# Kernel optimization log

Measured on AMD Instinct MI355X. Metric: run time of the kernel, lower is better.

Reference implementation:

```python
import jax, jax.numpy as jnp
import numpy as np

B, S, N, H, F, L, Lt = 2, 8, 150, 128, 40, 2, 1
EF = 2 * F + 2  # 82: src feat + dst feat + distance + bond
_rows_np, _cols_np = np.where(~np.eye(N, dtype=bool))  # fully connected, no self loops
_rows = jnp.asarray(_rows_np)
_cols = jnp.asarray(_cols_np)
E = _rows_np.shape[0]


def setup_inputs() -> dict:
    key = jax.random.key(0)
    ks = jax.random.split(key, 20)
    w = lambda k, shape: 0.1 * jax.random.normal(k, shape, dtype=jnp.float32)
    d = {}
    d['t'] = jax.random.uniform(ks[0], (B, 1), dtype=jnp.float32)
    d['x'] = jax.random.normal(ks[1], (B, S, N, 3), dtype=jnp.float32)
    d['peptide_seq'] = jax.random.randint(ks[2], (B, 15), 0, 20)
    d['atom_labels'] = jax.random.randint(ks[3], (B, N), 0, 5)
    d['amino_acid_pos'] = jax.random.randint(ks[4], (B, N), 1, 16)
    d['bond_matrix'] = (jax.random.uniform(ks[5], (B, N, N)) < 0.1).astype(jnp.float32)
    d['edge_mask'] = jnp.ones((B, N, N), jnp.float32)
    d['atom_mask'] = jnp.ones((B, N, 1), jnp.float32)
    d['restore_indices'] = jnp.tile(jnp.eye(N, dtype=jnp.float32)[None], (B, 1, 1))
    d['W_e1'] = w(ks[6], (L, EF, H)); d['b_e1'] = jnp.zeros((L, H), jnp.float32)
    d['W_e2'] = w(ks[7], (L, H, H)); d['b_e2'] = jnp.zeros((L, H), jnp.float32)
    d['W_c'] = w(ks[8], (L, H, 1)); d['b_c'] = jnp.zeros((L, 1), jnp.float32)
    d['W_h'] = w(ks[9], (L, F + H, F)); d['b_h'] = jnp.zeros((L, F), jnp.float32)
    d['w_t'] = w(ks[10], (L, 1, H)); d['w_b_t'] = jnp.zeros((L, H), jnp.float32)
    d['tW_e1'] = w(ks[11], (Lt, EF, H)); d['tb_e1'] = jnp.zeros((Lt, H), jnp.float32)
    d['tW_e2'] = w(ks[12], (Lt, H, H)); d['tb_e2'] = jnp.zeros((Lt, H), jnp.float32)
    d['tW_c'] = w(ks[13], (Lt, H, 1)); d['tb_c'] = jnp.zeros((Lt, 1), jnp.float32)
    d['tW_h'] = w(ks[14], (Lt, F + H, F)); d['tb_h'] = jnp.zeros((Lt, F), jnp.float32)
    return d


def _forward(t, x, peptide_seq, atom_labels, amino_acid_pos, bond_matrix, edge_mask,
             atom_mask, restore_indices, W_e1, b_e1, W_e2, b_e2, W_c, b_c, W_h, b_h,
             w_t, w_b_t, tW_e1, tb_e1, tW_e2, tb_e2, tW_c, tb_c, tW_h, tb_h):
    # single-atom embedding: [B, N, 40]
    aa = jnp.take_along_axis(peptide_seq, amino_acid_pos - 1, axis=1)
    emb = jnp.concatenate([
        jax.nn.one_hot(atom_labels, 5, dtype=x.dtype),
        jax.nn.one_hot(aa, 20, dtype=x.dtype),
        jax.nn.one_hot(amino_acid_pos - 1, 15, dtype=x.dtype)], axis=-1)
    h = jnp.broadcast_to(emb[:, None], (B, S, N, F))
    # restore absolute coordinates: x[b,s,i,d] = sum_j x[b,s,j,d] * R[b,i,j]
    x = jnp.einsum('bsjd,bij->bsid', x, restore_indices)
    x0 = x
    # per-edge masks/features (gathered once; identical math to full cdist + indexing)
    em_e = edge_mask.reshape(B, 1, N * N)[:, :, _rows * N + _cols][..., None]  # [B,1,E,1]
    bond_e = jnp.broadcast_to(bond_matrix[:, _rows, _cols][:, None, :, None], (B, S, E, 1))

    def layer(x, h, We1, be1, We2, be2, Wc, bc, Wh, bh, temb):
        diff = x[:, :, _rows] - x[:, :, _cols]                      # [B,S,E,3]
        dist = jnp.sqrt(jnp.sum(diff * diff, -1, keepdims=True) + 1e-12)
        ef = jnp.concatenate([h[:, :, _rows], h[:, :, _cols], dist, bond_e], -1)  # [B,S,E,82]
        m = jax.nn.silu(ef @ We1 + be1 + temb)
        m = jax.nn.silu(m @ We2 + be2) * em_e                        # [B,S,E,H]
        cw = m @ Wc + bc                                             # [B,S,E,1]
        x_out = jnp.zeros_like(x).at[:, :, _rows].add(diff * cw) / (N - 1)
        agg = jnp.zeros((B, S, N, m.shape[-1]), m.dtype).at[:, :, _rows].add(m)
        h_out = jax.nn.silu(jnp.concatenate([h, agg], -1) @ Wh + bh)
        return x_out, h_out

    for l in range(L):
        temb = (t @ w_t[l] + w_b_t[l])[:, None, None, :]             # [B,1,1,H]
        xo, h = layer(x, h, W_e1[l], b_e1[l], W_e2[l], b_e2[l], W_c[l], b_c[l], W_h[l], b_h[l], temb)
        x = x + xo
    for l in range(Lt):
        xo, h = layer(x, h, tW_e1[l], tb_e1[l], tW_e2[l], tb_e2[l], tW_c[l], tb_c[l], tW_h[l], tb_h[l], 0.0)
        x = x + xo
    return (x - x0) * atom_mask[:, None, :, :]


def reference(t, x, peptide_seq, atom_labels, amino_acid_pos, bond_matrix, edge_mask,
              atom_mask, restore_indices, W_e1, b_e1, W_e2, b_e2, W_c, b_c, W_h, b_h,
              w_t, w_b_t, tW_e1, tb_e1, tW_e2, tb_e2, tW_c, tb_c, tW_h, tb_h):
    return _forward(t, x, peptide_seq, atom_labels, amino_acid_pos, bond_matrix, edge_mask,
                    atom_mask, restore_indices, W_e1, b_e1, W_e2, b_e2, W_c, b_c, W_h, b_h,
                    w_t, w_b_t, tW_e1, tb_e1, tW_e2, tb_e2, tW_c, tb_c, tW_h, tb_h)
```

## Files before the change

### kernel.cpp

```cpp
#include <hip/hip_runtime.h>
#include <math.h>

#define B_ 2
#define S_ 8
#define N_ 150
#define H_ 128
#define F_ 40
#define EF_ 82
#define NP_ 160
#define MPQ 136

typedef __attribute__((ext_vector_type(8))) short short8;
typedef __attribute__((ext_vector_type(4))) float float4v;

__device__ __forceinline__ float silu_f(float v) {
    return v * __builtin_amdgcn_rcpf(1.0f + __expf(-v));
}

__device__ __forceinline__ unsigned short f2bf(float f) {
    unsigned u = __builtin_bit_cast(unsigned, f);
    return (unsigned short)((u + 0x7fffu + ((u >> 16) & 1u)) >> 16);
}

__global__ void prelude_kernel(const float* __restrict__ w0,
                               const float* __restrict__ w1,
                               const float* __restrict__ w2,
                               unsigned short* __restrict__ we2t,
                               const float* __restrict__ x,
                               const float* __restrict__ R,
                               float* __restrict__ xa,
                               float* __restrict__ x0,
                               const int* __restrict__ pep,
                               const int* __restrict__ labels,
                               const int* __restrict__ aapos,
                               const float* __restrict__ We1,
                               const float* __restrict__ be1,
                               const float* __restrict__ tp,
                               const float* __restrict__ wt,
                               const float* __restrict__ wbt,
                               float* __restrict__ h0,
                               float* __restrict__ Af,
                               float* __restrict__ Bf) {
    int bid = blockIdx.x;
    int tid = threadIdx.x;
    if (bid < 192) {
        int e = bid * 256 + tid;
        int l = e >> 14, idx = e & 16383;
        int k = idx >> 7, c = idx & 127;
        const float* src = (l == 0) ? w0 : (l == 1) ? w1 : w2;
        we2t[l * 16384 + c * H_ + k] = f2bf(src[idx]);
    } else if (bid < 221) {
        int idx = (bid - 192) * 256 + tid;
        if (idx < B_ * S_ * N_ * 3) {
            int d = idx % 3;
            int i = (idx / 3) % N_;
            int bs = idx / (3 * N_);
            int b = bs / S_;
            const float* xrow = x + bs * N_ * 3 + d;
            const float* Rrow = R + (b * N_ + i) * N_;
            float acc = 0.0f;
            for (int j = 0; j < N_; j++) acc += xrow[j * 3] * Rrow[j];
            xa[idx] = acc;
            x0[idx] = acc;
        }
    } else {
        int rel = bid - 221;
        int bi = rel * 2 + (tid >> 7);
        int b = bi / N_, i = bi % N_;
        int c = tid & 127;
        int al = labels[bi];
        int ap = aapos[bi];
        int aa = pep[b * 15 + ap - 1];
        int r0 = al, r1 = 5 + aa, r2 = 25 + ap - 1;
        float fa = We1[r0 * H_ + c] + We1[r1 * H_ + c] + We1[r2 * H_ + c]
                 + be1[c] + tp[b] * wt[c] + wbt[c];
        float fb = We1[(F_ + r0) * H_ + c] + We1[(F_ + r1) * H_ + c] + We1[(F_ + r2) * H_ + c];
        float hv = 0.0f;
        if (c < F_) hv = (c == r0 || c == r1 || c == r2) ? 1.0f : 0.0f;
        for (int s = 0; s < S_; s++) {
            int n = (b * S_ + s) * N_ + i;
            Af[n * H_ + c] = fa;
            Bf[n * H_ + c] = fb;
            if (c < F_) h0[n * F_ + c] = hv;
        }
    }
}

__global__ __launch_bounds__(256, 4) void edge_fused_kernel(
    const float* __restrict__ x_in,
    const float* __restrict__ Afeat,
    const float* __restrict__ Bfeat,
    const float* __restrict__ We1,
    const unsigned short* __restrict__ we2t,
    const float* __restrict__ be2,
    const float* __restrict__ Wc,
    const float* __restrict__ bcp,
    const float* __restrict__ bond,
    const float* __restrict__ emask,
    const float* __restrict__ h_in,
    const float* __restrict__ Wh,
    const float* __restrict__ bh,
    const float* __restrict__ We1n,
    const float* __restrict__ be1n,
    const float* __restrict__ tp,
    const float* __restrict__ wtn,
    const float* __restrict__ wbtn,
    int has_t,
    const float* __restrict__ x0v,
    const float* __restrict__ amask,
    int final_mode,
    float* __restrict__ x_out,
    float* __restrict__ h_out,
    float* __restrict__ Af_out,
    float* __restrict__ Bf_out)
{
    __shared__ __align__(16) short mbuf[2][16 * MPQ];
    __shared__ float4 diffE[NP_];
    __shared__ float2 dbL[NP_];
    __shared__ float DsumL[3];
    __shared__ float wpart[4][3];
    __shared__ float catL[F_ + H_];
    __shared__ float partL[120];
    __shared__ float hnewL[F_];

    int blk = blockIdx.x;
    int i = blk % N_, bs = blk / N_, b = bs / S_;
    int tid = threadIdx.x;
    int node = bs * N_ + i;
    int lane = tid & 63, w = tid >> 6;
    int qd = lane >> 4, l15 = lane & 15;
    int rowLoc = tid >> 4, c0 = (tid & 15) * 8;

    float xi0 = x_in[node * 3 + 0];
    float xi1 = x_in[node * 3 + 1];
    float xi2 = x_in[node * 3 + 2];

    if (tid < NP_) {
        int j = tid;
        float xj0 = xi0, xj1 = xi1, xj2 = xi2, bnd = 0.0f, emv = 0.0f;
        if (j < N_) {
            int nj = bs * N_ + j;
            xj0 = x_in[nj * 3 + 0];
            xj1 = x_in[nj * 3 + 1];
            xj2 = x_in[nj * 3 + 2];
            int eij = (b * N_ + i) * N_ + j;
            bnd = bond[eij];
            emv = (j == i) ? 0.0f : emask[eij];
        }
        float d0 = xi0 - xj0, d1 = xi1 - xj1, d2 = xi2 - xj2;
        diffE[j] = make_float4(d0, d1, d2, emv);
        dbL[j] = make_float2(sqrtf(d0 * d0 + d1 * d1 + d2 * d2 + 1e-12f), bnd);
    }

    float afr[8], w80r[8], w81r[8];
    {
        float4 t0 = *(const float4*)&Afeat[node * H_ + c0];
        float4 t1 = *(const float4*)&Afeat[node * H_ + c0 + 4];
        afr[0]=t0.x; afr[1]=t0.y; afr[2]=t0.z; afr[3]=t0.w;
        afr[4]=t1.x; afr[5]=t1.y; afr[6]=t1.z; afr[7]=t1.w;
        t0 = *(const float4*)&We1[80 * H_ + c0];
        t1 = *(const float4*)&We1[80 * H_ + c0 + 4];
        w80r[0]=t0.x; w80r[1]=t0.y; w80r[2]=t0.z; w80r[3]=t0.w;
        w80r[4]=t1.x; w80r[5]=t1.y; w80r[6]=t1.z; w80r[7]=t1.w;
        t0 = *(const float4*)&We1[81 * H_ + c0];
        t1 = *(const float4*)&We1[81 * H_ + c0 + 4];
        w81r[0]=t0.x; w81r[1]=t0.y; w81r[2]=t0.z; w81r[3]=t0.w;
        w81r[4]=t1.x; w81r[5]=t1.y; w81r[6]=t1.z; w81r[7]=t1.w;
    }

    int ctb = w * 2;
    float b2r0 = be2[ctb * 16 + l15],  b2r1 = be2[ctb * 16 + 16 + l15];
    float wc0  = Wc[ctb * 16 + l15],   wc1  = Wc[ctb * 16 + 16 + l15];
    const unsigned short* bb0 = we2t + (ctb * 16 + l15) * H_ + qd * 8;
    const unsigned short* bb1 = bb0 + 16 * H_;
    short8 bf00 = *(const short8*)(bb0 +  0);
    short8 bf01 = *(const short8*)(bb0 + 32);
    short8 bf02 = *(const short8*)(bb0 + 64);
    short8 bf03 = *(const short8*)(bb0 + 96);
    short8 bf10 = *(const short8*)(bb1 +  0);
    short8 bf11 = *(const short8*)(bb1 + 32);
    short8 bf12 = *(const short8*)(bb1 + 64);
    short8 bf13 = *(const short8*)(bb1 + 96);

    __syncthreads();

    if (w == 0) {
        float p0 = 0, p1 = 0, p2 = 0;
        for (int j = lane; j < NP_; j += 64) {
            float4 d = diffE[j];
            p0 += d.x; p1 += d.y; p2 += d.z;
        }
        for (int s = 1; s < 64; s <<= 1) {
            p0 += __shfl_xor(p0, s, 64);
            p1 += __shfl_xor(p1, s, 64);
            p2 += __shfl_xor(p2, s, 64);
        }
        if (lane == 0) { DsumL[0] = p0; DsumL[1] = p1; DsumL[2] = p2; }
    }

    float aggP0 = 0, aggP1 = 0;
    float SP00 = 0, SP01 = 0, SP02 = 0, SP10 = 0, SP11 = 0, SP12 = 0;

    for (int jt = 0; jt < 10; jt++) {
        short* mb = mbuf[jt & 1];
        int jrow = jt * 16 + rowLoc;
        float mv[8];
        if (jrow < N_) {
            const float* bp = &Bfeat[(bs * N_ + jrow) * H_ + c0];
            float4 b0 = *(const float4*)bp;
            float4 b1 = *(const float4*)(bp + 4);
            float br[8] = {b0.x, b0.y, b0.z, b0.w, b1.x, b1.y, b1.z, b1.w};
            float2 db = dbL[jrow];
#pragma unroll
            for (int u = 0; u < 8; u++)
                mv[u] = silu_f(afr[u] + br[u] + db.x * w80r[u] + db.y * w81r[u]);
        } else {
#pragma unroll
            for (int u = 0; u < 8; u++) mv[u] = 0.0f;
        }
        short8 pkv;
#pragma unroll
        for (int u = 0; u < 8; u++) pkv[u] = (short)f2bf(mv[u]);
        *(short8*)&mb[rowLoc * MPQ + c0] = pkv;
        __syncthreads();

        const short* arow = &mb[l15 * MPQ + qd * 8];
        short8 a0 = *(const short8*)(arow +  0);
        short8 a1 = *(const short8*)(arow + 32);
        short8 a2 = *(const short8*)(arow + 64);
        short8 a3 = *(const short8*)(arow + 96);
        float4v acc0 = {0, 0, 0, 0}, acc1 = {0, 0, 0, 0};
        acc0 = __builtin_amdgcn_mfma_f32_16x16x32_bf16(a0, bf00, acc0, 0, 0, 0);
        acc1 = __builtin_amdgcn_mfma_f32_16x16x32_bf16(a0, bf10, acc1, 0, 0, 0);
        acc0 = __builtin_amdgcn_mfma_f32_16x16x32_bf16(a1, bf01, acc0, 0, 0, 0);
        acc1 = __builtin_amdgcn_mfma_f32_16x16x32_bf16(a1, bf11, acc1, 0, 0, 0);
        acc0 = __builtin_amdgcn_mfma_f32_16x16x32_bf16(a2, bf02, acc0, 0, 0, 0);
        acc1 = __builtin_amdgcn_mfma_f32_16x16x32_bf16(a2, bf12, acc1, 0, 0, 0);
        acc0 = __builtin_amdgcn_mfma_f32_16x16x32_bf16(a3, bf03, acc0, 0, 0, 0);
        acc1 = __builtin_amdgcn_mfma_f32_16x16x32_bf16(a3, bf13, acc1, 0, 0, 0);

#pragma unroll
        for (int r = 0; r < 4; r++) {
            int j = jt * 16 + qd * 4 + r;
            float4 de = diffE[j];
            float mv0 = silu_f(acc0[r] + b2r0) * de.w;
            float mv1 = silu_f(acc1[r] + b2r1) * de.w;
            aggP0 += mv0; aggP1 += mv1;
            SP00 += de.x * mv0; SP01 += de.y * mv0; SP02 += de.z * mv0;
            SP10 += de.x * mv1; SP11 += de.y * mv1; SP12 += de.z * mv1;
        }
    }

#define QR_(v) { v += __shfl_xor(v, 16, 64); v += __shfl_xor(v, 32, 64); }
    QR_(aggP0) QR_(aggP1)
    QR_(SP00) QR_(SP01) QR_(SP02)
    QR_(SP10) QR_(SP11) QR_(SP12)
#undef QR_

    if (!final_mode) {
        if (qd == 0) {
            catL[F_ + ctb * 16 + l15]      = aggP0;
            catL[F_ + ctb * 16 + 16 + l15] = aggP1;
        }
        if (tid < F_) catL[tid] = h_in[node * F_ + tid];
    }

    float p0 = wc0 * SP00 + wc1 * SP10;
    float p1 = wc0 * SP01 + wc1 * SP11;
    float p2 = wc0 * SP02 + wc1 * SP12;
    for (int s = 1; s < 16; s <<= 1) {
        p0 += __shfl_xor(p0, s, 64);
        p1 += __shfl_xor(p1, s, 64);
        p2 += __shfl_xor(p2, s, 64);
    }
    if (lane == 0) { wpart[w][0] = p0; wpart[w][1] = p1; wpart[w][2] = p2; }
    __syncthreads();
    if (tid < 3) {
        float tot = wpart[0][tid] + wpart[1][tid] + wpart[2][tid] + wpart[3][tid]
                  + bcp[0] * DsumL[tid];
        float xn = x_in[node * 3 + tid] + tot * (1.0f / (float)(N_ - 1));
        if (final_mode)
            x_out[node * 3 + tid] = (xn - x0v[node * 3 + tid]) * amask[b * N_ + i];
        else
            x_out[node * 3 + tid] = xn;
    }

    if (final_mode) return;

    if (tid < 120) {
        int f = tid % 40, ks = tid / 40;
        float p = 0.0f;
        int k0 = ks * 56;
#pragma unroll 8
        for (int k = k0; k < k0 + 56; k++) p += catL[k] * Wh[k * F_ + f];
        partL[tid] = p;
    }
    __syncthreads();
    if (tid < F_) {
        float hv = silu_f(partL[tid] + partL[40 + tid] + partL[80 + tid] + bh[tid]);
        hnewL[tid] = hv;
        h_out[node * F_ + tid] = hv;
    }
    __syncthreads();
    if (tid < H_) {
        float fa = be1n[tid] + (has_t ? tp[b] * wtn[tid] + wbtn[tid] : 0.0f);
        float fb = 0.0f;
#pragma unroll 8
        for (int k = 0; k < F_; k++) {
            float hv = hnewL[k];
            fa += hv * We1n[k * H_ + tid];
            fb += hv * We1n[(F_ + k) * H_ + tid];
        }
        Af_out[node * H_ + tid] = fa;
        Bf_out[node * H_ + tid] = fb;
    }
}

extern "C" void kernel_launch(void* const* d_in, const int* in_sizes, int n_in,
                              void* d_out, int out_size, void* d_ws, size_t ws_size,
                              hipStream_t stream) {
    const float* t     = (const float*)d_in[0];
    const float* x     = (const float*)d_in[1];
    const int*   pep   = (const int*)d_in[2];
    const int*   labels= (const int*)d_in[3];
    const int*   aapos = (const int*)d_in[4];
    const float* bond  = (const float*)d_in[5];
    const float* em    = (const float*)d_in[6];
    const float* amask = (const float*)d_in[7];
    const float* R     = (const float*)d_in[8];
    const float* W_e1  = (const float*)d_in[9];
    const float* b_e1  = (const float*)d_in[10];
    const float* W_e2  = (const float*)d_in[11];
    const float* b_e2  = (const float*)d_in[12];
    const float* W_c   = (const float*)d_in[13];
    const float* b_c   = (const float*)d_in[14];
    const float* W_h   = (const float*)d_in[15];
    const float* b_h   = (const float*)d_in[16];
    const float* w_t   = (const float*)d_in[17];
    const float* w_b_t = (const float*)d_in[18];
    const float* tW_e1 = (const float*)d_in[19];
    const float* tb_e1 = (const float*)d_in[20];
    const float* tW_e2 = (const float*)d_in[21];
    const float* tb_e2 = (const float*)d_in[22];
    const float* tW_c  = (const float*)d_in[23];
    const float* tb_c  = (const float*)d_in[24];
    float* out = (float*)d_out;

    float* ws = (float*)d_ws;
    unsigned short* we2t = (unsigned short*)ws;
    float* x0  = ws + 24576;
    float* xA  = x0 + 7200;
    float* xB  = xA + 7200;
    float* hA  = xB + 7200;
    float* hB  = hA + 96000;
    float* Af1 = hB + 96000;
    float* Bf1 = Af1 + 307200;
    float* Af2 = Bf1 + 307200;
    float* Bf2 = Af2 + 307200;

    const int NB = B_ * S_ * N_;

    prelude_kernel<<<371, 256, 0, stream>>>(W_e2, W_e2 + H_ * H_, tW_e2, we2t,
                                            x, R, xA, x0,
                                            pep, labels, aapos, W_e1, b_e1,
                                            t, w_t, w_b_t, hA, Af1, Bf1);

    edge_fused_kernel<<<NB, 256, 0, stream>>>(
        xA, Af1, Bf1, W_e1, we2t, b_e2, W_c, b_c, bond, em,
        hA, W_h, b_h, W_e1 + EF_ * H_, b_e1 + H_, t, w_t + H_, w_b_t + H_, 1,
        nullptr, nullptr, 0,
        xB, hB, Af2, Bf2);

    edge_fused_kernel<<<NB, 256, 0, stream>>>(
        xB, Af2, Bf2, W_e1 + EF_ * H_, we2t + 16384, b_e2 + H_, W_c + H_, b_c + 1,
        bond, em,
        hB, W_h + (F_ + H_) * F_, b_h + F_, tW_e1, tb_e1, nullptr, nullptr, nullptr, 0,
        nullptr, nullptr, 0,
        xA, hA, Af1, Bf1);

    edge_fused_kernel<<<NB, 256, 0, stream>>>(
        xA, Af1, Bf1, tW_e1, we2t + 32768, tb_e2, tW_c, tb_c, bond, em,
        nullptr, nullptr, nullptr, nullptr, nullptr, nullptr, nullptr, nullptr, 0,
        x0, amask, 1,
        out, nullptr, nullptr, nullptr);
}
```

Measured before the change: 269.9 us.

## Fuse all layers into cooperative mega-kernel and process two nodes per block

Merges the prelude and three edge-layer kernels into one cooperative kernel that separates stages with grid-wide syncs. When cooperative launch is unavailable or the occupancy check fails, it falls back to separate launches. Each block now handles two destination nodes, which halves the block count and lets the shared W_e2 B-fragments and the Bfeat rows be reused for both nodes. Launch bounds go up to 5 blocks per SM. The cost is more registers and shared memory per block, plus grid-sync overhead. A 1200-block grid may also fail the residency check.

```diff
diff --git a/kernel.cpp b/kernel.cpp
--- a/kernel.cpp
+++ b/kernel.cpp
@@ -1,4 +1,5 @@
 #include <hip/hip_runtime.h>
+#include <hip/hip_cooperative_groups.h>
 #include <math.h>
 
 #define B_ 2
@@ -9,6 +10,10 @@
 #define EF_ 82
 #define NP_ 160
 #define MPQ 136
+#define NPAIR 75
+#define GRID2 1200
+
+namespace cg = cooperative_groups;
 
 typedef __attribute__((ext_vector_type(8))) short short8;
 typedef __attribute__((ext_vector_type(4))) float float4v;
@@ -22,32 +27,32 @@
     return (unsigned short)((u + 0x7fffu + ((u >> 16) & 1u)) >> 16);
 }
 
-__global__ void prelude_kernel(const float* __restrict__ w0,
-                               const float* __restrict__ w1,
-                               const float* __restrict__ w2,
-                               unsigned short* __restrict__ we2t,
-                               const float* __restrict__ x,
-                               const float* __restrict__ R,
-                               float* __restrict__ xa,
-                               float* __restrict__ x0,
-                               const int* __restrict__ pep,
-                               const int* __restrict__ labels,
-                               const int* __restrict__ aapos,
-                               const float* __restrict__ We1,
-                               const float* __restrict__ be1,
-                               const float* __restrict__ tp,
-                               const float* __restrict__ wt,
-                               const float* __restrict__ wbt,
-                               float* __restrict__ h0,
-                               float* __restrict__ Af,
-                               float* __restrict__ Bf) {
+__device__ void prelude_dev(const float* __restrict__ W_e2,
+                            const float* __restrict__ tW_e2,
+                            unsigned short* __restrict__ we2t,
+                            const float* __restrict__ x,
+                            const float* __restrict__ R,
+                            float* __restrict__ xa,
+                            float* __restrict__ x0,
+                            const int* __restrict__ pep,
+                            const int* __restrict__ labels,
+                            const int* __restrict__ aapos,
+                            const float* __restrict__ We1,
+                            const float* __restrict__ be1,
+                            const float* __restrict__ tp,
+                            const float* __restrict__ wt,
+                            const float* __restrict__ wbt,
+                            float* __restrict__ h0,
+                            float* __restrict__ Af,
+                            float* __restrict__ Bf)
+{
     int bid = blockIdx.x;
     int tid = threadIdx.x;
     if (bid < 192) {
         int e = bid * 256 + tid;
         int l = e >> 14, idx = e & 16383;
         int k = idx >> 7, c = idx & 127;
-        const float* src = (l == 0) ? w0 : (l == 1) ? w1 : w2;
+        const float* src = (l == 0) ? W_e2 : (l == 1) ? (W_e2 + H_ * H_) : tW_e2;
         we2t[l * 16384 + c * H_ + k] = f2bf(src[idx]);
     } else if (bid < 221) {
         int idx = (bid - 192) * 256 + tid;
@@ -63,7 +68,7 @@
             xa[idx] = acc;
             x0[idx] = acc;
         }
-    } else {
+    } else if (bid < 371) {
         int rel = bid - 221;
         int bi = rel * 2 + (tid >> 7);
         int b = bi / N_, i = bi % N_;
@@ -86,12 +91,12 @@
     }
 }
 
-__global__ __launch_bounds__(256, 4) void edge_fused_kernel(
+__device__ void edge2_dev(
     const float* __restrict__ x_in,
     const float* __restrict__ Afeat,
     const float* __restrict__ Bfeat,
     const float* __restrict__ We1,
-    const unsigned short* __restrict__ we2t,
+    const unsigned short* __restrict__ we2p,
     const float* __restrict__ be2,
     const float* __restrict__ Wc,
     const float* __restrict__ bcp,
@@ -114,50 +119,69 @@
     float* __restrict__ Af_out,
     float* __restrict__ Bf_out)
 {
-    __shared__ __align__(16) short mbuf[2][16 * MPQ];
-    __shared__ float4 diffE[NP_];
-    __shared__ float2 dbL[NP_];
-    __shared__ float DsumL[3];
-    __shared__ float wpart[4][3];
-    __shared__ float catL[F_ + H_];
-    __shared__ float partL[120];
-    __shared__ float hnewL[F_];
+    __shared__ __align__(16) short mbuf[2][2][16 * MPQ];
+    __shared__ float4 diffE[2][NP_];
+    __shared__ float2 dbL[2][NP_];
+    __shared__ float DsumL[2][3];
+    __shared__ float wpart[2][4][3];
+    __shared__ float catL[2][F_ + H_];
+    __shared__ float partL[2][120];
+    __shared__ float hnewL[2][F_];
 
     int blk = blockIdx.x;
-    int i = blk % N_, bs = blk / N_, b = bs / S_;
+    int bs = blk / NPAIR;
+    int pr = blk % NPAIR;
+    int i0 = pr * 2, i1 = i0 + 1;
+    int b = bs / S_;
     int tid = threadIdx.x;
-    int node = bs * N_ + i;
+    int nodeA = bs * N_ + i0, nodeB = nodeA + 1;
     int lane = tid & 63, w = tid >> 6;
     int qd = lane >> 4, l15 = lane & 15;
     int rowLoc = tid >> 4, c0 = (tid & 15) * 8;
 
-    float xi0 = x_in[node * 3 + 0];
-    float xi1 = x_in[node * 3 + 1];
-    float xi2 = x_in[node * 3 + 2];
+    float xiA0 = x_in[nodeA * 3 + 0];
+    float xiA1 = x_in[nodeA * 3 + 1];
+    float xiA2 = x_in[nodeA * 3 + 2];
+    float xiB0 = x_in[nodeB * 3 + 0];
+    float xiB1 = x_in[nodeB * 3 + 1];
+    float xiB2 = x_in[nodeB * 3 + 2];
 
     if (tid < NP_) {
         int j = tid;
-        float xj0 = xi0, xj1 = xi1, xj2 = xi2, bnd = 0.0f, emv = 0.0f;
         if (j < N_) {
             int nj = bs * N_ + j;
-            xj0 = x_in[nj * 3 + 0];
-            xj1 = x_in[nj * 3 + 1];
-            xj2 = x_in[nj * 3 + 2];
-            int eij = (b * N_ + i) * N_ + j;
-            bnd = bond[eij];
-            emv = (j == i) ? 0.0f : emask[eij];
-        }
-        float d0 = xi0 - xj0, d1 = xi1 - xj1, d2 = xi2 - xj2;
-        diffE[j] = make_float4(d0, d1, d2, emv);
-        dbL[j] = make_float2(sqrtf(d0 * d0 + d1 * d1 + d2 * d2 + 1e-12f), bnd);
-    }
-
-    float afr[8], w80r[8], w81r[8];
+            float xj0 = x_in[nj * 3 + 0];
+            float xj1 = x_in[nj * 3 + 1];
+            float xj2 = x_in[nj * 3 + 2];
+            int eA = (b * N_ + i0) * N_ + j;
+            int eB = eA + N_;
+            float bndA = bond[eA], bndB = bond[eB];
+            float emA = (j == i0) ? 0.0f : emask[eA];
+            float emB = (j == i1) ? 0.0f : emask[eB];
+            float dA0 = xiA0 - xj0, dA1 = xiA1 - xj1, dA2 = xiA2 - xj2;
+            float dB0 = xiB0 - xj0, dB1 = xiB1 - xj1, dB2 = xiB2 - xj2;
+            diffE[0][j] = make_float4(dA0, dA1, dA2, emA);
+            diffE[1][j] = make_float4(dB0, dB1, dB2, emB);
+            dbL[0][j] = make_float2(sqrtf(dA0*dA0 + dA1*dA1 + dA2*dA2 + 1e-12f), bndA);
+            dbL[1][j] = make_float2(sqrtf(dB0*dB0 + dB1*dB1 + dB2*dB2 + 1e-12f), bndB);
+        } else {
+            diffE[0][j] = make_float4(0.f, 0.f, 0.f, 0.f);
+            diffE[1][j] = make_float4(0.f, 0.f, 0.f, 0.f);
+            dbL[0][j] = make_float2(0.f, 0.f);
+            dbL[1][j] = make_float2(0.f, 0.f);
+        }
+    }
+
+    float afrA[8], afrB[8], w80r[8], w81r[8];
     {
-        float4 t0 = *(const float4*)&Afeat[node * H_ + c0];
-        float4 t1 = *(const float4*)&Afeat[node * H_ + c0 + 4];
-        afr[0]=t0.x; afr[1]=t0.y; afr[2]=t0.z; afr[3]=t0.w;
-        afr[4]=t1.x; afr[5]=t1.y; afr[6]=t1.z; afr[7]=t1.w;
+        float4 t0 = *(const float4*)&Afeat[nodeA * H_ + c0];
+        float4 t1 = *(const float4*)&Afeat[nodeA * H_ + c0 + 4];
+        afrA[0]=t0.x; afrA[1]=t0.y; afrA[2]=t0.z; afrA[3]=t0.w;
+        afrA[4]=t1.x; afrA[5]=t1.y; afrA[6]=t1.z; afrA[7]=t1.w;
+        t0 = *(const float4*)&Afeat[nodeB * H_ + c0];
+        t1 = *(const float4*)&Afeat[nodeB * H_ + c0 + 4];
+        afrB[0]=t0.x; afrB[1]=t0.y; afrB[2]=t0.z; afrB[3]=t0.w;
+        afrB[4]=t1.x; afrB[5]=t1.y; afrB[6]=t1.z; afrB[7]=t1.w;
         t0 = *(const float4*)&We1[80 * H_ + c0];
         t1 = *(const float4*)&We1[80 * H_ + c0 + 4];
         w80r[0]=t0.x; w80r[1]=t0.y; w80r[2]=t0.z; w80r[3]=t0.w;
@@ -171,7 +195,7 @@
     int ctb = w * 2;
     float b2r0 = be2[ctb * 16 + l15],  b2r1 = be2[ctb * 16 + 16 + l15];
     float wc0  = Wc[ctb * 16 + l15],   wc1  = Wc[ctb * 16 + 16 + l15];
-    const unsigned short* bb0 = we2t + (ctb * 16 + l15) * H_ + qd * 8;
+    const unsigned short* bb0 = we2p + (ctb * 16 + l15) * H_ + qd * 8;
     const unsigned short* bb1 = bb0 + 16 * H_;
     short8 bf00 = *(const short8*)(bb0 +  0);
     short8 bf01 = *(const short8*)(bb0 + 32);
@@ -184,10 +208,10 @@
 
     __syncthreads();
 
-    if (w == 0) {
+    if (w < 2) {
         float p0 = 0, p1 = 0, p2 = 0;
         for (int j = lane; j < NP_; j += 64) {
-            float4 d = diffE[j];
+            float4 d = diffE[w][j];
             p0 += d.x; p1 += d.y; p2 += d.z;
         }
         for (int s = 1; s < 64; s <<= 1) {
@@ -195,125 +219,239 @@
             p1 += __shfl_xor(p1, s, 64);
             p2 += __shfl_xor(p2, s, 64);
         }
-        if (lane == 0) { DsumL[0] = p0; DsumL[1] = p1; DsumL[2] = p2; }
-    }
-
-    float aggP0 = 0, aggP1 = 0;
-    float SP00 = 0, SP01 = 0, SP02 = 0, SP10 = 0, SP11 = 0, SP12 = 0;
+        if (lane == 0) { DsumL[w][0] = p0; DsumL[w][1] = p1; DsumL[w][2] = p2; }
+    }
+
+    float agA0 = 0, agA1 = 0, agB0 = 0, agB1 = 0;
+    float SA00 = 0, SA01 = 0, SA02 = 0, SA10 = 0, SA11 = 0, SA12 = 0;
+    float SB00 = 0, SB01 = 0, SB02 = 0, SB10 = 0, SB11 = 0, SB12 = 0;
 
     for (int jt = 0; jt < 10; jt++) {
-        short* mb = mbuf[jt & 1];
+        short* mbA = mbuf[jt & 1][0];
+        short* mbB = mbuf[jt & 1][1];
         int jrow = jt * 16 + rowLoc;
-        float mv[8];
+        float mvA[8], mvB[8];
         if (jrow < N_) {
             const float* bp = &Bfeat[(bs * N_ + jrow) * H_ + c0];
             float4 b0 = *(const float4*)bp;
             float4 b1 = *(const float4*)(bp + 4);
             float br[8] = {b0.x, b0.y, b0.z, b0.w, b1.x, b1.y, b1.z, b1.w};
-            float2 db = dbL[jrow];
+            float2 dA = dbL[0][jrow];
+            float2 dB = dbL[1][jrow];
 #pragma unroll
-            for (int u = 0; u < 8; u++)
-                mv[u] = silu_f(afr[u] + br[u] + db.x * w80r[u] + db.y * w81r[u]);
+            for (int u = 0; u < 8; u++) {
+                mvA[u] = silu_f(afrA[u] + br[u] + dA.x * w80r[u] + dA.y * w81r[u]);
+                mvB[u] = silu_f(afrB[u] + br[u] + dB.x * w80r[u] + dB.y * w81r[u]);
+            }
         } else {
 #pragma unroll
-            for (int u = 0; u < 8; u++) mv[u] = 0.0f;
-        }
-        short8 pkv;
+            for (int u = 0; u < 8; u++) { mvA[u] = 0.0f; mvB[u] = 0.0f; }
+        }
+        short8 pkA, pkB;
 #pragma unroll
-        for (int u = 0; u < 8; u++) pkv[u] = (short)f2bf(mv[u]);
-        *(short8*)&mb[rowLoc * MPQ + c0] = pkv;
+        for (int u = 0; u < 8; u++) { pkA[u] = (short)f2bf(mvA[u]); pkB[u] = (short)f2bf(mvB[u]); }
+        *(short8*)&mbA[rowLoc * MPQ + c0] = pkA;
+        *(short8*)&mbB[rowLoc * MPQ + c0] = pkB;
         __syncthreads();
 
-        const short* arow = &mb[l15 * MPQ + qd * 8];
-        short8 a0 = *(const short8*)(arow +  0);
-        short8 a1 = *(const short8*)(arow + 32);
-        short8 a2 = *(const short8*)(arow + 64);
-        short8 a3 = *(const short8*)(arow + 96);
-        float4v acc0 = {0, 0, 0, 0}, acc1 = {0, 0, 0, 0};
-        acc0 = __builtin_amdgcn_mfma_f32_16x16x32_bf16(a0, bf00, acc0, 0, 0, 0);
-        acc1 = __builtin_amdgcn_mfma_f32_16x16x32_bf16(a0, bf10, acc1, 0, 0, 0);
-        acc0 = __builtin_amdgcn_mfma_f32_16x16x32_bf16(a1, bf01, acc0, 0, 0, 0);
-        acc1 = __builtin_amdgcn_mfma_f32_16x16x32_bf16(a1, bf11, acc1, 0, 0, 0);
-        acc0 = __builtin_amdgcn_mfma_f32_16x16x32_bf16(a2, bf02, acc0, 0, 0, 0);
-        acc1 = __builtin_amdgcn_mfma_f32_16x16x32_bf16(a2, bf12, acc1, 0, 0, 0);
-        acc0 = __builtin_amdgcn_mfma_f32_16x16x32_bf16(a3, bf03, acc0, 0, 0, 0);
-        acc1 = __builtin_amdgcn_mfma_f32_16x16x32_bf16(a3, bf13, acc1, 0, 0, 0);
+        const short* arA = &mbA[l15 * MPQ + qd * 8];
+        const short* arB = &mbB[l15 * MPQ + qd * 8];
+        short8 aA0 = *(const short8*)(arA +  0);
+        short8 aA1 = *(const short8*)(arA + 32);
+        short8 aA2 = *(const short8*)(arA + 64);
+        short8 aA3 = *(const short8*)(arA + 96);
+        short8 aB0 = *(const short8*)(arB +  0);
+        short8 aB1 = *(const short8*)(arB + 32);
+        short8 aB2 = *(const short8*)(arB + 64);
+        short8 aB3 = *(const short8*)(arB + 96);
+        float4v accA0 = {0, 0, 0, 0}, accA1 = {0, 0, 0, 0};
+        float4v accB0 = {0, 0, 0, 0}, accB1 = {0, 0, 0, 0};
+        accA0 = __builtin_amdgcn_mfma_f32_16x16x32_bf16(aA0, bf00, accA0, 0, 0, 0);
+        accB0 = __builtin_amdgcn_mfma_f32_16x16x32_bf16(aB0, bf00, accB0, 0, 0, 0);
+        accA1 = __builtin_amdgcn_mfma_f32_16x16x32_bf16(aA0, bf10, accA1, 0, 0, 0);
+        accB1 = __builtin_amdgcn_mfma_f32_16x16x32_bf16(aB0, bf10, accB1, 0, 0, 0);
+        accA0 = __builtin_amdgcn_mfma_f32_16x16x32_bf16(aA1, bf01, accA0, 0, 0, 0);
+        accB0 = __builtin_amdgcn_mfma_f32_16x16x32_bf16(aB1, bf01, accB0, 0, 0, 0);
+        accA1 = __builtin_amdgcn_mfma_f32_16x16x32_bf16(aA1, bf11, accA1, 0, 0, 0);
+        accB1 = __builtin_amdgcn_mfma_f32_16x16x32_bf16(aB1, bf11, accB1, 0, 0, 0);
+        accA0 = __builtin_amdgcn_mfma_f32_16x16x32_bf16(aA2, bf02, accA0, 0, 0, 0);
+        accB0 = __builtin_amdgcn_mfma_f32_16x16x32_bf16(aB2, bf02, accB0, 0, 0, 0);
+        accA1 = __builtin_amdgcn_mfma_f32_16x16x32_bf16(aA2, bf12, accA1, 0, 0, 0);
+        accB1 = __builtin_amdgcn_mfma_f32_16x16x32_bf16(aB2, bf12, accB1, 0, 0, 0);
+        accA0 = __builtin_amdgcn_mfma_f32_16x16x32_bf16(aA3, bf03, accA0, 0, 0, 0);
+        accB0 = __builtin_amdgcn_mfma_f32_16x16x32_bf16(aB3, bf03, accB0, 0, 0, 0);
+        accA1 = __builtin_amdgcn_mfma_f32_16x16x32_bf16(aA3, bf13, accA1, 0, 0, 0);
+        accB1 = __builtin_amdgcn_mfma_f32_16x16x32_bf16(aB3, bf13, accB1, 0, 0, 0);
 
 #pragma unroll
         for (int r = 0; r < 4; r++) {
             int j = jt * 16 + qd * 4 + r;
-            float4 de = diffE[j];
-            float mv0 = silu_f(acc0[r] + b2r0) * de.w;
-            float mv1 = silu_f(acc1[r] + b2r1) * de.w;
-            aggP0 += mv0; aggP1 += mv1;
-            SP00 += de.x * mv0; SP01 += de.y * mv0; SP02 += de.z * mv0;
-            SP10 += de.x * mv1; SP11 += de.y * mv1; SP12 += de.z * mv1;
+            float4 deA = diffE[0][j];
+            float4 deB = diffE[1][j];
+            float mA0 = silu_f(accA0[r] + b2r0) * deA.w;
+            float mA1 = silu_f(accA1[r] + b2r1) * deA.w;
+            float mB0 = silu_f(accB0[r] + b2r0) * deB.w;
+            float mB1 = silu_f(accB1[r] + b2r1) * deB.w;
+            agA0 += mA0; agA1 += mA1; agB0 += mB0; agB1 += mB1;
+            SA00 += deA.x * mA0; SA01 += deA.y * mA0; SA02 += deA.z * mA0;
+            SA10 += deA.x * mA1; SA11 += deA.y * mA1; SA12 += deA.z * mA1;
+            SB00 += deB.x * mB0; SB01 += deB.y * mB0; SB02 += deB.z * mB0;
+            SB10 += deB.x * mB1; SB11 += deB.y * mB1; SB12 += deB.z * mB1;
         }
     }
 
 #define QR_(v) { v += __shfl_xor(v, 16, 64); v += __shfl_xor(v, 32, 64); }
-    QR_(aggP0) QR_(aggP1)
-    QR_(SP00) QR_(SP01) QR_(SP02)
-    QR_(SP10) QR_(SP11) QR_(SP12)
+    QR_(agA0) QR_(agA1) QR_(agB0) QR_(agB1)
+    QR_(SA00) QR_(SA01) QR_(SA02) QR_(SA10) QR_(SA11) QR_(SA12)
+    QR_(SB00) QR_(SB01) QR_(SB02) QR_(SB10) QR_(SB11) QR_(SB12)
 #undef QR_
 
     if (!final_mode) {
         if (qd == 0) {
-            catL[F_ + ctb * 16 + l15]      = aggP0;
-            catL[F_ + ctb * 16 + 16 + l15] = aggP1;
-        }
-        if (tid < F_) catL[tid] = h_in[node * F_ + tid];
-    }
-
-    float p0 = wc0 * SP00 + wc1 * SP10;
-    float p1 = wc0 * SP01 + wc1 * SP11;
-    float p2 = wc0 * SP02 + wc1 * SP12;
+            catL[0][F_ + ctb * 16 + l15]      = agA0;
+            catL[0][F_ + ctb * 16 + 16 + l15] = agA1;
+            catL[1][F_ + ctb * 16 + l15]      = agB0;
+            catL[1][F_ + ctb * 16 + 16 + l15] = agB1;
+        }
+        if (tid < F_) catL[0][tid] = h_in[nodeA * F_ + tid];
+        else if (tid >= 128 && tid < 128 + F_) catL[1][tid - 128] = h_in[nodeB * F_ + (tid - 128)];
+    }
+
+    float pA0 = wc0 * SA00 + wc1 * SA10;
+    float pA1 = wc0 * SA01 + wc1 * SA11;
+    float pA2 = wc0 * SA02 + wc1 * SA12;
+    float pB0 = wc0 * SB00 + wc1 * SB10;
+    float pB1 = wc0 * SB01 + wc1 * SB11;
+    float pB2 = wc0 * SB02 + wc1 * SB12;
     for (int s = 1; s < 16; s <<= 1) {
-        p0 += __shfl_xor(p0, s, 64);
-        p1 += __shfl_xor(p1, s, 64);
-        p2 += __shfl_xor(p2, s, 64);
-    }
-    if (lane == 0) { wpart[w][0] = p0; wpart[w][1] = p1; wpart[w][2] = p2; }
+        pA0 += __shfl_xor(pA0, s, 64);
+        pA1 += __shfl_xor(pA1, s, 64);
+        pA2 += __shfl_xor(pA2, s, 64);
+        pB0 += __shfl_xor(pB0, s, 64);
+        pB1 += __shfl_xor(pB1, s, 64);
+        pB2 += __shfl_xor(pB2, s, 64);
+    }
+    if (lane == 0) {
+        wpart[0][w][0] = pA0; wpart[0][w][1] = pA1; wpart[0][w][2] = pA2;
+        wpart[1][w][0] = pB0; wpart[1][w][1] = pB1; wpart[1][w][2] = pB2;
+    }
     __syncthreads();
     if (tid < 3) {
-        float tot = wpart[0][tid] + wpart[1][tid] + wpart[2][tid] + wpart[3][tid]
-                  + bcp[0] * DsumL[tid];
-        float xn = x_in[node * 3 + tid] + tot * (1.0f / (float)(N_ - 1));
+        float tot = wpart[0][0][tid] + wpart[0][1][tid] + wpart[0][2][tid] + wpart[0][3][tid]
+                  + bcp[0] * DsumL[0][tid];
+        float xn = x_in[nodeA * 3 + tid] + tot * (1.0f / (float)(N_ - 1));
         if (final_mode)
-            x_out[node * 3 + tid] = (xn - x0v[node * 3 + tid]) * amask[b * N_ + i];
+            x_out[nodeA * 3 + tid] = (xn - x0v[nodeA * 3 + tid]) * amask[b * N_ + i0];
         else
-            x_out[node * 3 + tid] = xn;
+            x_out[nodeA * 3 + tid] = xn;
+    } else if (tid >= 64 && tid < 67) {
+        int d = tid - 64;
+        float tot = wpart[1][0][d] + wpart[1][1][d] + wpart[1][2][d] + wpart[1][3][d]
+                  + bcp[0] * DsumL[1][d];
+        float xn = x_in[nodeB * 3 + d] + tot * (1.0f / (float)(N_ - 1));
+        if (final_mode)
+            x_out[nodeB * 3 + d] = (xn - x0v[nodeB * 3 + d]) * amask[b * N_ + i1];
+        else
+            x_out[nodeB * 3 + d] = xn;
     }
 
     if (final_mode) return;
 
-    if (tid < 120) {
-        int f = tid % 40, ks = tid / 40;
+    int half = tid >> 7;
+    int lt = tid & 127;
+    int nodeT = half ? nodeB : nodeA;
+    if (lt < 120) {
+        int f = lt % 40, ks = lt / 40;
         float p = 0.0f;
         int k0 = ks * 56;
 #pragma unroll 8
-        for (int k = k0; k < k0 + 56; k++) p += catL[k] * Wh[k * F_ + f];
-        partL[tid] = p;
+        for (int k = k0; k < k0 + 56; k++) p += catL[half][k] * Wh[k * F_ + f];
+        partL[half][lt] = p;
     }
     __syncthreads();
-    if (tid < F_) {
-        float hv = silu_f(partL[tid] + partL[40 + tid] + partL[80 + tid] + bh[tid]);
-        hnewL[tid] = hv;
-        h_out[node * F_ + tid] = hv;
+    if (lt < F_) {
+        float hv = silu_f(partL[half][lt] + partL[half][40 + lt] + partL[half][80 + lt] + bh[lt]);
+        hnewL[half][lt] = hv;
+        h_out[nodeT * F_ + lt] = hv;
     }
     __syncthreads();
-    if (tid < H_) {
-        float fa = be1n[tid] + (has_t ? tp[b] * wtn[tid] + wbtn[tid] : 0.0f);
+    {
+        float fa = be1n[lt] + (has_t ? tp[b] * wtn[lt] + wbtn[lt] : 0.0f);
         float fb = 0.0f;
 #pragma unroll 8
         for (int k = 0; k < F_; k++) {
-            float hv = hnewL[k];
-            fa += hv * We1n[k * H_ + tid];
-            fb += hv * We1n[(F_ + k) * H_ + tid];
-        }
-        Af_out[node * H_ + tid] = fa;
-        Bf_out[node * H_ + tid] = fb;
-    }
+            float hv = hnewL[half][k];
+            fa += hv * We1n[k * H_ + lt];
+            fb += hv * We1n[(F_ + k) * H_ + lt];
+        }
+        Af_out[nodeT * H_ + lt] = fa;
+        Bf_out[nodeT * H_ + lt] = fb;
+    }
+}
+
+__global__ void prelude_kernel(const float* W_e2, const float* tW_e2,
+                               unsigned short* we2t,
+                               const float* x, const float* R,
+                               float* xa, float* x0,
+                               const int* pep, const int* labels, const int* aapos,
+                               const float* We1, const float* be1,
+                               const float* tp, const float* wt, const float* wbt,
+                               float* h0, float* Af, float* Bf) {
+    prelude_dev(W_e2, tW_e2, we2t, x, R, xa, x0, pep, labels, aapos,
+                We1, be1, tp, wt, wbt, h0, Af, Bf);
+}
+
+__global__ __launch_bounds__(256, 5) void edge2_kernel(
+    const float* x_in, const float* Afeat, const float* Bfeat,
+    const float* We1, const unsigned short* we2p, const float* be2,
+    const float* Wc, const float* bcp, const float* bond, const float* emask,
+    const float* h_in, const float* Wh, const float* bh,
+    const float* We1n, const float* be1n,
+    const float* tp, const float* wtn, const float* wbtn, int has_t,
+    const float* x0v, const float* amask, int final_mode,
+    float* x_out, float* h_out, float* Af_out, float* Bf_out) {
+    edge2_dev(x_in, Afeat, Bfeat, We1, we2p, be2, Wc, bcp, bond, emask,
+              h_in, Wh, bh, We1n, be1n, tp, wtn, wbtn, has_t,
+              x0v, amask, final_mode, x_out, h_out, Af_out, Bf_out);
+}
+
+__global__ __launch_bounds__(256, 5) void mega_kernel(
+    const float* W_e2, const float* tW_e2, unsigned short* we2t,
+    const float* x, const float* R, float* xA, float* x0,
+    const int* pep, const int* labels, const int* aapos,
+    const float* W_e1, const float* b_e1,
+    const float* tvec, const float* w_t, const float* w_b_t,
+    float* hA, float* Af1, float* Bf1,
+    const float* b_e2, const float* W_c, const float* b_c,
+    const float* W_h, const float* b_h,
+    const float* tW_e1, const float* tb_e1, const float* tb_e2,
+    const float* tW_c, const float* tb_c,
+    const float* bond, const float* em, const float* amask,
+    float* xB, float* hB, float* Af2, float* Bf2, float* out)
+{
+    cg::grid_group grid = cg::this_grid();
+
+    prelude_dev(W_e2, tW_e2, we2t, x, R, xA, x0, pep, labels, aapos,
+                W_e1, b_e1, tvec, w_t, w_b_t, hA, Af1, Bf1);
+    grid.sync();
+
+    edge2_dev(xA, Af1, Bf1, W_e1, we2t, b_e2, W_c, b_c, bond, em,
+              hA, W_h, b_h, W_e1 + EF_ * H_, b_e1 + H_,
+              tvec, w_t + H_, w_b_t + H_, 1,
+              nullptr, nullptr, 0, xB, hB, Af2, Bf2);
+    grid.sync();
+
+    edge2_dev(xB, Af2, Bf2, W_e1 + EF_ * H_, we2t + 16384, b_e2 + H_,
+              W_c + H_, b_c + 1, bond, em,
+              hB, W_h + (F_ + H_) * F_, b_h + F_, tW_e1, tb_e1,
+              nullptr, nullptr, nullptr, 0,
+              nullptr, nullptr, 0, xA, hA, Af1, Bf1);
+    grid.sync();
+
+    edge2_dev(xA, Af1, Bf1, tW_e1, we2t + 32768, tb_e2, tW_c, tb_c, bond, em,
+              nullptr, nullptr, nullptr, nullptr, nullptr,
+              nullptr, nullptr, nullptr, 0,
+              x0, amask, 1, out, nullptr, nullptr, nullptr);
 }
 
 extern "C" void kernel_launch(void* const* d_in, const int* in_sizes, int n_in,
@@ -358,29 +496,59 @@
     float* Af2 = Bf1 + 307200;
     float* Bf2 = Af2 + 307200;
 
-    const int NB = B_ * S_ * N_;
-
-    prelude_kernel<<<371, 256, 0, stream>>>(W_e2, W_e2 + H_ * H_, tW_e2, we2t,
-                                            x, R, xA, x0,
-                                            pep, labels, aapos, W_e1, b_e1,
-                                            t, w_t, w_b_t, hA, Af1, Bf1);
-
-    edge_fused_kernel<<<NB, 256, 0, stream>>>(
-        xA, Af1, Bf1, W_e1, we2t, b_e2, W_c, b_c, bond, em,
-        hA, W_h, b_h, W_e1 + EF_ * H_, b_e1 + H_, t, w_t + H_, w_b_t + H_, 1,
-        nullptr, nullptr, 0,
-        xB, hB, Af2, Bf2);
-
-    edge_fused_kernel<<<NB, 256, 0, stream>>>(
-        xB, Af2, Bf2, W_e1 + EF_ * H_, we2t + 16384, b_e2 + H_, W_c + H_, b_c + 1,
-        bond, em,
-        hB, W_h + (F_ + H_) * F_, b_h + F_, tW_e1, tb_e1, nullptr, nullptr, nullptr, 0,
-        nullptr, nullptr, 0,
-        xA, hA, Af1, Bf1);
-
-    edge_fused_kernel<<<NB, 256, 0, stream>>>(
-        xA, Af1, Bf1, tW_e1, we2t + 32768, tb_e2, tW_c, tb_c, bond, em,
-        nullptr, nullptr, nullptr, nullptr, nullptr, nullptr, nullptr, nullptr, 0,
-        x0, amask, 1,
-        out, nullptr, nullptr, nullptr);
-}
+    static int coop_state = -1;
+    if (coop_state < 0) {
+        int nb = 0;
+        hipError_t e1 = hipOccupancyMaxActiveBlocksPerMultiprocessor(
+            &nb, reinterpret_cast<const void*>(mega_kernel), 256, 0);
+        hipDeviceProp_t prop;
+        int dev = 0;
+        hipGetDevice(&dev);
+        hipError_t e2 = hipGetDeviceProperties(&prop, dev);
+        coop_state = (e1 == hipSuccess && e2 == hipSuccess &&
+                      prop.cooperativeLaunch &&
+                      (long)nb * prop.multiProcessorCount >= GRID2) ? 1 : 0;
+    }
+
+    bool launched = false;
+    if (coop_state == 1) {
+        void* args[] = {
+            (void*)&W_e2, (void*)&tW_e2, (void*)&we2t,
+            (void*)&x, (void*)&R, (void*)&xA, (void*)&x0,
+            (void*)&pep, (void*)&labels, (void*)&aapos,
+            (void*)&W_e1, (void*)&b_e1,
+            (void*)&t, (void*)&w_t, (void*)&w_b_t,
+            (void*)&hA, (void*)&Af1, (void*)&Bf1,
+            (void*)&b_e2, (void*)&W_c, (void*)&b_c,
+            (void*)&W_h, (void*)&b_h,
+            (void*)&tW_e1, (void*)&tb_e1, (void*)&tb_e2,
+            (void*)&tW_c, (void*)&tb_c,
+            (void*)&bond, (void*)&em, (void*)&amask,
+            (void*)&xB, (void*)&hB, (void*)&Af2, (void*)&Bf2, (void*)&out
+        };
+        hipError_t e = hipLaunchCooperativeKernel(
+            reinterpret_cast<const void*>(mega_kernel),
+            dim3(GRID2), dim3(256), args, 0, stream);
+        launched = (e == hipSuccess);
+        if (!launched) coop_state = 0;
+    }
+
+    if (!launched) {
+        prelude_kernel<<<371, 256, 0, stream>>>(W_e2, tW_e2, we2t, x, R, xA, x0,
+                                                pep, labels, aapos, W_e1, b_e1,
+                                                t, w_t, w_b_t, hA, Af1, Bf1);
+        edge2_kernel<<<GRID2, 256, 0, stream>>>(
+            xA, Af1, Bf1, W_e1, we2t, b_e2, W_c, b_c, bond, em,
+            hA, W_h, b_h, W_e1 + EF_ * H_, b_e1 + H_, t, w_t + H_, w_b_t + H_, 1,
+            nullptr, nullptr, 0, xB, hB, Af2, Bf2);
+        edge2_kernel<<<GRID2, 256, 0, stream>>>(
+            xB, Af2, Bf2, W_e1 + EF_ * H_, we2t + 16384, b_e2 + H_, W_c + H_, b_c + 1,
+            bond, em, hB, W_h + (F_ + H_) * F_, b_h + F_, tW_e1, tb_e1,
+            nullptr, nullptr, nullptr, 0,
+            nullptr, nullptr, 0, xA, hA, Af1, Bf1);
+        edge2_kernel<<<GRID2, 256, 0, stream>>>(
+            xA, Af1, Bf1, tW_e1, we2t + 32768, tb_e2, tW_c, tb_c, bond, em,
+            nullptr, nullptr, nullptr, nullptr, nullptr, nullptr, nullptr, nullptr, 0,
+            x0, amask, 1, out, nullptr, nullptr, nullptr);
+    }
+}
```

Result: slower. 424.2 us (+57.2%).
